# Optimization experiments

Measured on AMD Instinct MI355X. Metric: run time of the kernel, lower is better.

## Reference

```python
import jax, jax.numpy as jnp
import numpy as np


def _gskan_layer(x, Lam, eps, a):
    # x: [B, n_in], Lam: [n_in, n_out], eps: [n_out], a: scalar PReLU weight
    s = x[:, :, None] + eps  # [B, n_in, n_out] broadcast add
    act = jnp.where(s >= 0, s, a * s)  # PReLU with single shared parameter
    return jnp.einsum('bpq,pq->bq', act, Lam)  # weighted sum over n_in


def setup_inputs() -> dict:
    key = jax.random.key(0)
    B, input_dim, width, depth, output_dim = 1024, 256, 512, 3, 256
    dims = [input_dim] + [width] * depth + [output_dim]
    ks = jax.random.split(key, 1 + 2 * (len(dims) - 1))
    inp = {"x": jax.random.normal(ks[0], (B, input_dim), dtype=jnp.float32)}
    for i in range(len(dims) - 1):
        n_in, n_out = dims[i], dims[i + 1]
        inp[f"L{i}_Lambda"] = 0.02 * jax.random.normal(ks[1 + 2 * i], (n_in, n_out), dtype=jnp.float32)
        inp[f"L{i}_eps"] = 0.02 * jax.random.normal(ks[2 + 2 * i], (n_out,), dtype=jnp.float32)
        inp[f"L{i}_a"] = jnp.float32(0.25)  # PReLU default init
    return inp


def reference(x,
              L0_Lambda, L0_eps, L0_a,
              L1_Lambda, L1_eps, L1_a,
              L2_Lambda, L2_eps, L2_a,
              L3_Lambda, L3_eps, L3_a):
    params = [(L0_Lambda, L0_eps, L0_a), (L1_Lambda, L1_eps, L1_a),
              (L2_Lambda, L2_eps, L2_a), (L3_Lambda, L3_eps, L3_a)]
    for Lam, eps, a in params:
        x = _gskan_layer(x, Lam, eps, a)
    return x
```

## Files before the change

kernel.cpp:

```cpp
#include <hip/hip_runtime.h>


#define PCHUNK 64

__global__ __launch_bounds__(256) void gskan_partial_kernel(
    const float* __restrict__ X,
    const float* __restrict__ Lam,
    const float* __restrict__ Eps,
    const float* __restrict__ Aw,
    float* __restrict__ Part,
    int B, int n_in, int n_out, int p_per_split)
{
    __shared__ float xs[64][PCHUNK + 4];
    __shared__ float ls[PCHUNK][64];

    const int tid = threadIdx.x;
    const int qg  = tid & 15;
    const int bl  = tid >> 4;

    const int q0 = blockIdx.x * 64;
    const int b0 = blockIdx.y * 64;
    const int p_begin = blockIdx.z * p_per_split;
    int p_end = p_begin + p_per_split;
    if (p_end > n_in) p_end = n_in;

    const float a  = Aw[0];
    const float c1 = 0.5f * (1.0f + a);
    const float c2 = 0.5f * (1.0f - a);

    const int q = q0 + qg * 4;
    const float4 epsv = *reinterpret_cast<const float4*>(Eps + q);
    const float ee[4] = {epsv.x, epsv.y, epsv.z, epsv.w};

    float acc1[4][4] = {};
    float acc2[4][4] = {};

    for (int pc = p_begin; pc < p_end; pc += PCHUNK) {
        #pragma unroll
        for (int r = 0; r < 4; ++r) {
            int slot = r * 256 + tid;
            int row  = slot >> 4;
            int c4   = slot & 15;
            float4 v = *reinterpret_cast<const float4*>(
                X + (size_t)(b0 + row) * n_in + pc + c4 * 4);
            *reinterpret_cast<float4*>(&xs[row][c4 * 4]) = v;
        }
        #pragma unroll
        for (int r = 0; r < 4; ++r) {
            int slot = r * 256 + tid;
            int row  = slot >> 4;
            int c4   = slot & 15;
            float4 v = *reinterpret_cast<const float4*>(
                Lam + (size_t)(pc + row) * n_out + q0 + c4 * 4);
            *reinterpret_cast<float4*>(&ls[row][c4 * 4]) = v;
        }
        __syncthreads();

        for (int p = 0; p < PCHUNK; p += 4) {
            float4 xv[4];
            #pragma unroll
            for (int i = 0; i < 4; ++i)
                xv[i] = *reinterpret_cast<const float4*>(&xs[bl * 4 + i][p]);

            #pragma unroll
            for (int pp = 0; pp < 4; ++pp) {
                float4 lv = *reinterpret_cast<const float4*>(&ls[p + pp][qg * 4]);
                const float le[4] = {lv.x, lv.y, lv.z, lv.w};
                #pragma unroll
                for (int i = 0; i < 4; ++i) {
                    const float xe = (pp == 0) ? xv[i].x :
                                     (pp == 1) ? xv[i].y :
                                     (pp == 2) ? xv[i].z : xv[i].w;
                    #pragma unroll
                    for (int j = 0; j < 4; ++j) {
                        const float s = xe + ee[j];
                        acc1[i][j] = fmaf(s,        le[j], acc1[i][j]);
                        acc2[i][j] = fmaf(fabsf(s), le[j], acc2[i][j]);
                    }
                }
            }
        }
        __syncthreads();
    }

    float* P = Part + (size_t)blockIdx.z * B * n_out;
    #pragma unroll
    for (int i = 0; i < 4; ++i) {
        const int b = b0 + bl * 4 + i;
        float4 o;
        o.x = c1 * acc1[i][0] + c2 * acc2[i][0];
        o.y = c1 * acc1[i][1] + c2 * acc2[i][1];
        o.z = c1 * acc1[i][2] + c2 * acc2[i][2];
        o.w = c1 * acc1[i][3] + c2 * acc2[i][3];
        *reinterpret_cast<float4*>(P + (size_t)b * n_out + q) = o;
    }
}

__global__ __launch_bounds__(256) void gskan_combine_kernel(
    const float* __restrict__ Part, float* __restrict__ Y, int n, int nsplit)
{
    int i = (blockIdx.x * 256 + threadIdx.x) * 4;
    if (i >= n) return;
    float4 acc = *reinterpret_cast<const float4*>(Part + i);
    for (int s = 1; s < nsplit; ++s) {
        float4 v = *reinterpret_cast<const float4*>(Part + (size_t)s * n + i);
        acc.x += v.x; acc.y += v.y; acc.z += v.z; acc.w += v.w;
    }
    *reinterpret_cast<float4*>(Y + i) = acc;
}

extern "C" void kernel_launch(void* const* d_in, const int* in_sizes, int n_in_args,
                              void* d_out, int out_size, void* d_ws, size_t ws_size,
                              hipStream_t stream)
{
    (void)n_in_args; (void)out_size;

    const float* x = (const float*)d_in[0];

    struct LayerP { const float *Lam, *Eps, *Aw; int n_in, n_out; };
    LayerP layers[4];
    for (int i = 0; i < 4; ++i) {
        layers[i].Lam   = (const float*)d_in[1 + 3 * i];
        layers[i].Eps   = (const float*)d_in[2 + 3 * i];
        layers[i].Aw    = (const float*)d_in[3 + 3 * i];
        layers[i].n_out = in_sizes[2 + 3 * i];
        layers[i].n_in  = in_sizes[1 + 3 * i] / layers[i].n_out;
    }
    const int B = in_sizes[0] / layers[0].n_in;

    char* ws = (char*)d_ws;
    float* Part = (float*)ws;
    float* yA   = (float*)(ws + (size_t)(8u << 20));
    float* yB   = (float*)(ws + (size_t)(10u << 20));
    const bool have_ws = ws_size >= (size_t)(12u << 20);

    const float* cur = x;
    for (int i = 0; i < 4; ++i) {
        const LayerP& ly = layers[i];
        const int nq = ly.n_out / 64;
        const int nb = B / 64;

        int nsplit = 1;
        if (have_ws) {
            nsplit = 512 / (nq * nb);
            if (nsplit < 1) nsplit = 1;
            int max_split = ly.n_in / PCHUNK;
            if (nsplit > max_split) nsplit = max_split;
        }
        int p_per = ((ly.n_in + nsplit * PCHUNK - 1) / (nsplit * PCHUNK)) * PCHUNK;
        nsplit = (ly.n_in + p_per - 1) / p_per;

        float* Y = (i == 3) ? (float*)d_out : ((i % 2 == 0) ? yA : yB);
        float* dst = (nsplit == 1) ? Y : Part;

        dim3 grid(nq, nb, nsplit), block(256);
        hipLaunchKernelGGL(gskan_partial_kernel, grid, block, 0, stream,
                           cur, ly.Lam, ly.Eps, ly.Aw, dst,
                           B, ly.n_in, ly.n_out, p_per);

        if (nsplit > 1) {
            const int n = B * ly.n_out;
            dim3 cg((n / 4 + 255) / 256), cb(256);
            hipLaunchKernelGGL(gskan_combine_kernel, cg, cb, 0, stream, Part, Y, n, nsplit);
        }
        cur = Y;
    }
}
```

Measured before the change: 115.4 us.

## Enlarge batch tile to 128 rows with 8x4 per-thread micro-tile and swizzled LDS

Doubles the batch tile per block to 128 rows, so each thread accumulates an 8x4 output tile instead of 4x4. This improves register reuse of the Lambda values per LDS load. The p-chunk is halved to 32 to keep shared memory small. The X tile is stored with an XOR swizzle to avoid LDS bank conflicts, and the workspace layout is enlarged to hold more split partials. The trade-off is higher register pressure (64 accumulators), fewer blocks per layer and more split partial traffic, which could lower occupancy.

```diff
diff --git a/kernel.cpp b/kernel.cpp
--- a/kernel.cpp
+++ b/kernel.cpp
@@ -1,7 +1,7 @@
 #include <hip/hip_runtime.h>
 
 
-#define PCHUNK 64
+#define PCHUNK 32
 
 __global__ __launch_bounds__(256) void gskan_partial_kernel(
     const float* __restrict__ X,
@@ -11,15 +11,15 @@
     float* __restrict__ Part,
     int B, int n_in, int n_out, int p_per_split)
 {
-    __shared__ float xs[64][PCHUNK + 4];
-    __shared__ float ls[PCHUNK][64];
+    __shared__ float xs[128 * PCHUNK];
+    __shared__ float ls[PCHUNK * 64];
 
     const int tid = threadIdx.x;
     const int qg  = tid & 15;
     const int bl  = tid >> 4;
 
     const int q0 = blockIdx.x * 64;
-    const int b0 = blockIdx.y * 64;
+    const int b0 = blockIdx.y * 128;
     const int p_begin = blockIdx.z * p_per_split;
     int p_end = p_begin + p_per_split;
     if (p_end > n_in) p_end = n_in;
@@ -29,51 +29,53 @@
     const float c2 = 0.5f * (1.0f - a);
 
     const int q = q0 + qg * 4;
-    const float4 epsv = *reinterpret_cast<const float4*>(Eps + q);
-    const float ee[4] = {epsv.x, epsv.y, epsv.z, epsv.w};
+    const float4 ev = *reinterpret_cast<const float4*>(Eps + q);
+    const float ee[4] = {ev.x, ev.y, ev.z, ev.w};
 
-    float acc1[4][4] = {};
-    float acc2[4][4] = {};
+    float acc1[8][4] = {};
+    float acc2[8][4] = {};
 
     for (int pc = p_begin; pc < p_end; pc += PCHUNK) {
         #pragma unroll
         for (int r = 0; r < 4; ++r) {
             int slot = r * 256 + tid;
-            int row  = slot >> 4;
-            int c4   = slot & 15;
+            int row  = slot >> 3;
+            int pg   = slot & 7;
             float4 v = *reinterpret_cast<const float4*>(
-                X + (size_t)(b0 + row) * n_in + pc + c4 * 4);
-            *reinterpret_cast<float4*>(&xs[row][c4 * 4]) = v;
+                X + (size_t)(b0 + row) * n_in + pc + pg * 4);
+            int spg = pg ^ ((row >> 3) & 3);
+            *reinterpret_cast<float4*>(&xs[row * PCHUNK + spg * 4]) = v;
         }
         #pragma unroll
-        for (int r = 0; r < 4; ++r) {
+        for (int r = 0; r < 2; ++r) {
             int slot = r * 256 + tid;
             int row  = slot >> 4;
             int c4   = slot & 15;
             float4 v = *reinterpret_cast<const float4*>(
                 Lam + (size_t)(pc + row) * n_out + q0 + c4 * 4);
-            *reinterpret_cast<float4*>(&ls[row][c4 * 4]) = v;
+            *reinterpret_cast<float4*>(&ls[row * 64 + c4 * 4]) = v;
         }
         __syncthreads();
 
+        #pragma unroll
         for (int p = 0; p < PCHUNK; p += 4) {
-            float4 xv[4];
+            float4 lv[4];
             #pragma unroll
-            for (int i = 0; i < 4; ++i)
-                xv[i] = *reinterpret_cast<const float4*>(&xs[bl * 4 + i][p]);
-
+            for (int pp = 0; pp < 4; ++pp)
+                lv[pp] = *reinterpret_cast<const float4*>(&ls[(p + pp) * 64 + qg * 4]);
+            const int pg = p >> 2;
             #pragma unroll
-            for (int pp = 0; pp < 4; ++pp) {
-                float4 lv = *reinterpret_cast<const float4*>(&ls[p + pp][qg * 4]);
-                const float le[4] = {lv.x, lv.y, lv.z, lv.w};
+            for (int i = 0; i < 8; ++i) {
+                const int row = bl * 8 + i;
+                const int spg = pg ^ ((row >> 3) & 3);
+                float4 xv = *reinterpret_cast<const float4*>(&xs[row * PCHUNK + spg * 4]);
+                const float xe[4] = {xv.x, xv.y, xv.z, xv.w};
                 #pragma unroll
-                for (int i = 0; i < 4; ++i) {
-                    const float xe = (pp == 0) ? xv[i].x :
-                                     (pp == 1) ? xv[i].y :
-                                     (pp == 2) ? xv[i].z : xv[i].w;
+                for (int pp = 0; pp < 4; ++pp) {
+                    const float le[4] = {lv[pp].x, lv[pp].y, lv[pp].z, lv[pp].w};
                     #pragma unroll
                     for (int j = 0; j < 4; ++j) {
-                        const float s = xe + ee[j];
+                        const float s = xe[pp] + ee[j];
                         acc1[i][j] = fmaf(s,        le[j], acc1[i][j]);
                         acc2[i][j] = fmaf(fabsf(s), le[j], acc2[i][j]);
                     }
@@ -85,8 +87,8 @@
 
     float* P = Part + (size_t)blockIdx.z * B * n_out;
     #pragma unroll
-    for (int i = 0; i < 4; ++i) {
-        const int b = b0 + bl * 4 + i;
+    for (int i = 0; i < 8; ++i) {
+        const int b = b0 + bl * 8 + i;
         float4 o;
         o.x = c1 * acc1[i][0] + c2 * acc2[i][0];
         o.y = c1 * acc1[i][1] + c2 * acc2[i][1];
@@ -130,15 +132,15 @@
 
     char* ws = (char*)d_ws;
     float* Part = (float*)ws;
-    float* yA   = (float*)(ws + (size_t)(8u << 20));
-    float* yB   = (float*)(ws + (size_t)(10u << 20));
-    const bool have_ws = ws_size >= (size_t)(12u << 20);
+    float* yA   = (float*)(ws + (size_t)(16u << 20));
+    float* yB   = (float*)(ws + (size_t)(18u << 20));
+    const bool have_ws = ws_size >= (size_t)(20u << 20);
 
     const float* cur = x;
     for (int i = 0; i < 4; ++i) {
         const LayerP& ly = layers[i];
         const int nq = ly.n_out / 64;
-        const int nb = B / 64;
+        const int nb = B / 128;
 
         int nsplit = 1;
         if (have_ws) {
```

Result: slower. 144.2 us (+25.0%).

## Widen output tile to 128 columns with 4x8 per-thread register blocking

Applied to the files above, without the earlier changes.

Each block now covers 128 output columns instead of 64, and each thread accumulates a 4x8 tile. The input chunk along n_in is halved to 32 so shared memory stays small, and launch bounds request 4 blocks per CU. The aim is more arithmetic per shared-memory load and fewer blocks re-reading the same X rows. In exchange it raises register pressure and leaves fewer tiles, so more split-K partials and a larger workspace are needed: the have_ws threshold rises to 20 MB, and if the workspace is smaller the split-K path is turned off.

```diff
diff --git a/kernel.cpp b/kernel.cpp
--- a/kernel.cpp
+++ b/kernel.cpp
@@ -1,9 +1,10 @@
 #include <hip/hip_runtime.h>
 
 
-#define PCHUNK 64
+#define PCHUNK 32
+#define XS_STRIDE 36
 
-__global__ __launch_bounds__(256) void gskan_partial_kernel(
+__global__ __launch_bounds__(256, 4) void gskan_partial_kernel(
     const float* __restrict__ X,
     const float* __restrict__ Lam,
     const float* __restrict__ Eps,
@@ -11,14 +12,14 @@
     float* __restrict__ Part,
     int B, int n_in, int n_out, int p_per_split)
 {
-    __shared__ float xs[64][PCHUNK + 4];
-    __shared__ float ls[PCHUNK][64];
+    __shared__ float xs[64 * XS_STRIDE];
+    __shared__ float ls[PCHUNK * 128];
 
     const int tid = threadIdx.x;
     const int qg  = tid & 15;
     const int bl  = tid >> 4;
 
-    const int q0 = blockIdx.x * 64;
+    const int q0 = blockIdx.x * 128;
     const int b0 = blockIdx.y * 64;
     const int p_begin = blockIdx.z * p_per_split;
     int p_end = p_begin + p_per_split;
@@ -28,44 +29,51 @@
     const float c1 = 0.5f * (1.0f + a);
     const float c2 = 0.5f * (1.0f - a);
 
-    const int q = q0 + qg * 4;
-    const float4 epsv = *reinterpret_cast<const float4*>(Eps + q);
-    const float ee[4] = {epsv.x, epsv.y, epsv.z, epsv.w};
+    float ee[8];
+    {
+        float4 eA = *reinterpret_cast<const float4*>(Eps + q0 + qg * 4);
+        float4 eB = *reinterpret_cast<const float4*>(Eps + q0 + 64 + qg * 4);
+        ee[0] = eA.x; ee[1] = eA.y; ee[2] = eA.z; ee[3] = eA.w;
+        ee[4] = eB.x; ee[5] = eB.y; ee[6] = eB.z; ee[7] = eB.w;
+    }
 
-    float acc1[4][4] = {};
-    float acc2[4][4] = {};
+    float acc1[4][8] = {};
+    float acc2[4][8] = {};
 
     for (int pc = p_begin; pc < p_end; pc += PCHUNK) {
         #pragma unroll
-        for (int r = 0; r < 4; ++r) {
+        for (int r = 0; r < 2; ++r) {
             int slot = r * 256 + tid;
-            int row  = slot >> 4;
-            int c4   = slot & 15;
+            int row  = slot >> 3;
+            int pg   = slot & 7;
             float4 v = *reinterpret_cast<const float4*>(
-                X + (size_t)(b0 + row) * n_in + pc + c4 * 4);
-            *reinterpret_cast<float4*>(&xs[row][c4 * 4]) = v;
+                X + (size_t)(b0 + row) * n_in + pc + pg * 4);
+            *reinterpret_cast<float4*>(&xs[row * XS_STRIDE + pg * 4]) = v;
         }
         #pragma unroll
         for (int r = 0; r < 4; ++r) {
             int slot = r * 256 + tid;
-            int row  = slot >> 4;
-            int c4   = slot & 15;
+            int row  = slot >> 5;
+            int c4   = slot & 31;
             float4 v = *reinterpret_cast<const float4*>(
                 Lam + (size_t)(pc + row) * n_out + q0 + c4 * 4);
-            *reinterpret_cast<float4*>(&ls[row][c4 * 4]) = v;
+            *reinterpret_cast<float4*>(&ls[row * 128 + c4 * 4]) = v;
         }
         __syncthreads();
 
+        #pragma unroll 2
         for (int p = 0; p < PCHUNK; p += 4) {
             float4 xv[4];
             #pragma unroll
             for (int i = 0; i < 4; ++i)
-                xv[i] = *reinterpret_cast<const float4*>(&xs[bl * 4 + i][p]);
+                xv[i] = *reinterpret_cast<const float4*>(&xs[(bl * 4 + i) * XS_STRIDE + p]);
 
             #pragma unroll
             for (int pp = 0; pp < 4; ++pp) {
-                float4 lv = *reinterpret_cast<const float4*>(&ls[p + pp][qg * 4]);
-                const float le[4] = {lv.x, lv.y, lv.z, lv.w};
+                float4 lA = *reinterpret_cast<const float4*>(&ls[(p + pp) * 128 + qg * 4]);
+                float4 lB = *reinterpret_cast<const float4*>(&ls[(p + pp) * 128 + 64 + qg * 4]);
+                const float la[4] = {lA.x, lA.y, lA.z, lA.w};
+                const float lb[4] = {lB.x, lB.y, lB.z, lB.w};
                 #pragma unroll
                 for (int i = 0; i < 4; ++i) {
                     const float xe = (pp == 0) ? xv[i].x :
@@ -73,9 +81,12 @@
                                      (pp == 2) ? xv[i].z : xv[i].w;
                     #pragma unroll
                     for (int j = 0; j < 4; ++j) {
-                        const float s = xe + ee[j];
-                        acc1[i][j] = fmaf(s,        le[j], acc1[i][j]);
-                        acc2[i][j] = fmaf(fabsf(s), le[j], acc2[i][j]);
+                        const float sA = xe + ee[j];
+                        acc1[i][j]     = fmaf(sA,        la[j], acc1[i][j]);
+                        acc2[i][j]     = fmaf(fabsf(sA), la[j], acc2[i][j]);
+                        const float sB = xe + ee[4 + j];
+                        acc1[i][4 + j] = fmaf(sB,        lb[j], acc1[i][4 + j]);
+                        acc2[i][4 + j] = fmaf(fabsf(sB), lb[j], acc2[i][4 + j]);
                     }
                 }
             }
@@ -87,12 +98,17 @@
     #pragma unroll
     for (int i = 0; i < 4; ++i) {
         const int b = b0 + bl * 4 + i;
-        float4 o;
-        o.x = c1 * acc1[i][0] + c2 * acc2[i][0];
-        o.y = c1 * acc1[i][1] + c2 * acc2[i][1];
-        o.z = c1 * acc1[i][2] + c2 * acc2[i][2];
-        o.w = c1 * acc1[i][3] + c2 * acc2[i][3];
-        *reinterpret_cast<float4*>(P + (size_t)b * n_out + q) = o;
+        float4 oA, oB;
+        oA.x = c1 * acc1[i][0] + c2 * acc2[i][0];
+        oA.y = c1 * acc1[i][1] + c2 * acc2[i][1];
+        oA.z = c1 * acc1[i][2] + c2 * acc2[i][2];
+        oA.w = c1 * acc1[i][3] + c2 * acc2[i][3];
+        oB.x = c1 * acc1[i][4] + c2 * acc2[i][4];
+        oB.y = c1 * acc1[i][5] + c2 * acc2[i][5];
+        oB.z = c1 * acc1[i][6] + c2 * acc2[i][6];
+        oB.w = c1 * acc1[i][7] + c2 * acc2[i][7];
+        *reinterpret_cast<float4*>(P + (size_t)b * n_out + q0 + qg * 4) = oA;
+        *reinterpret_cast<float4*>(P + (size_t)b * n_out + q0 + 64 + qg * 4) = oB;
     }
 }
 
@@ -130,14 +146,14 @@
 
     char* ws = (char*)d_ws;
     float* Part = (float*)ws;
-    float* yA   = (float*)(ws + (size_t)(8u << 20));
-    float* yB   = (float*)(ws + (size_t)(10u << 20));
-    const bool have_ws = ws_size >= (size_t)(12u << 20);
+    float* yA   = (float*)(ws + (size_t)(16u << 20));
+    float* yB   = (float*)(ws + (size_t)(18u << 20));
+    const bool have_ws = ws_size >= (size_t)(20u << 20);
 
     const float* cur = x;
     for (int i = 0; i < 4; ++i) {
         const LayerP& ly = layers[i];
-        const int nq = ly.n_out / 64;
+        const int nq = ly.n_out / 128;
         const int nb = B / 64;
 
         int nsplit = 1;
```

After: 185.8 us. 1.61x slower.
